# Kernel tuning notes

Measured on AMD Instinct MI355X. Metric: run time of the kernel, lower is better.

Reference implementation:

```python
import jax, jax.numpy as jnp
import numpy as np

HIDDEN = 2048
N_HEADS = 16
N_KV = 4
HEAD_DIM = 128
THETA = 500000.0
FREQ_ALLOC = 20  # t section; h = w = (HEAD_DIM//2 - 20)//2 = 22
T = 2048


def setup_inputs() -> dict:
    key = jax.random.key(0)
    k1, k2, k3, k4 = jax.random.split(key, 4)
    positions = jax.random.randint(k1, (3, T), 0, 1024, dtype=jnp.int32)
    hidden_states = jax.random.normal(k2, (T, HIDDEN), dtype=jnp.float32)
    w_qkv = jax.random.normal(k3, (HIDDEN, (N_HEADS + 2 * N_KV) * HEAD_DIM), dtype=jnp.float32) * 0.02
    w_o = jax.random.normal(k4, (N_HEADS * HEAD_DIM, HIDDEN), dtype=jnp.float32) * 0.02
    return {"positions": positions, "hidden_states": hidden_states, "w_qkv": w_qkv, "w_o": w_o}


def _mrope_cos_sin(positions):
    # standard rope table evaluated at positions: cos/sin each [3, T, HEAD_DIM//2]
    inv_freq = 1.0 / (THETA ** (jnp.arange(0, HEAD_DIM, 2, dtype=jnp.float32) / HEAD_DIM))
    freqs = positions.astype(jnp.float32)[..., None] * inv_freq
    cos, sin = jnp.cos(freqs), jnp.sin(freqs)
    sh = (HEAD_DIM // 2 - FREQ_ALLOC) // 2  # 22

    def section(c):
        c_t = c[0, :, -FREQ_ALLOC:]          # time dims from t-positions
        c_h = c[1, :, 0:2 * sh:2]            # even low-freq dims from h-positions
        c_w = c[2, :, 1:2 * sh:2]            # odd low-freq dims from w-positions
        c_hw = jnp.stack([c_h, c_w], axis=-1).reshape(c_h.shape[0], 2 * sh)
        return jnp.concatenate([c_hw, c_t], axis=-1)  # [T, HEAD_DIM//2]

    return section(cos), section(sin)


def _rotate_interleaved(x, cos, sin):
    # is_neox_style=False: even/odd interleaved rotation. x: [T, H, HEAD_DIM]
    x1, x2 = x[..., 0::2], x[..., 1::2]
    c, s = cos[:, None, :], sin[:, None, :]
    o1 = x1 * c - x2 * s
    o2 = x2 * c + x1 * s
    return jnp.stack([o1, o2], axis=-1).reshape(x.shape)


def reference(positions, hidden_states, w_qkv, w_o):
    q_size = N_HEADS * HEAD_DIM
    kv_size = N_KV * HEAD_DIM
    qkv = hidden_states @ w_qkv  # [T, 3072]
    q = qkv[:, :q_size].reshape(T, N_HEADS, HEAD_DIM)
    k = qkv[:, q_size:q_size + kv_size].reshape(T, N_KV, HEAD_DIM)
    v = qkv[:, q_size + kv_size:].reshape(T, N_KV, HEAD_DIM)

    cos, sin = _mrope_cos_sin(positions)
    q = _rotate_interleaved(q, cos, sin)
    k = _rotate_interleaved(k, cos, sin)

    # GQA causal attention
    rep = N_HEADS // N_KV
    kr = jnp.repeat(k, rep, axis=1)  # [T, N_HEADS, D]
    vr = jnp.repeat(v, rep, axis=1)
    scale = HEAD_DIM ** -0.5
    scores = jnp.einsum('qhd,khd->hqk', q, kr) * scale
    causal = jnp.tril(jnp.ones((T, T), dtype=bool))
    scores = jnp.where(causal[None], scores, jnp.finfo(scores.dtype).min)
    attn = jax.nn.softmax(scores, axis=-1)
    out = jnp.einsum('hqk,khd->qhd', attn, vr).reshape(T, N_HEADS * HEAD_DIM)
    return out @ w_o
```

## Files before the change

### kernel.cpp

```cpp
#include <hip/hip_runtime.h>
#include <math.h>

#define T 2048
#define HIDDEN 2048
#define NH 16
#define NKV 4
#define HD 128
#define QKV_N 3072
#define Q_SIZE 2048
#define KV_SIZE 512

typedef __attribute__((ext_vector_type(8))) short short8;
typedef __attribute__((ext_vector_type(4))) short short4v;
typedef __attribute__((ext_vector_type(4))) float floatx4;
typedef __attribute__((ext_vector_type(16))) float floatx16;

#define VMCNT(N) asm volatile("s_waitcnt vmcnt(" #N ")" ::: "memory")
#define LGKMCNT0 asm volatile("s_waitcnt lgkmcnt(0)" ::: "memory")
#define BARRIER_RAW()                          \
    do {                                       \
        __builtin_amdgcn_s_barrier();          \
        asm volatile("" ::: "memory");         \
    } while (0)

__device__ __forceinline__ unsigned short f2bf(float f) {
    union { float f; unsigned int u; } v; v.f = f;
    unsigned int u = v.u;
    u += 0x7fffu + ((u >> 16) & 1u);
    return (unsigned short)(u >> 16);
}

__device__ __forceinline__ void gload_lds16(const unsigned short* g, unsigned short* l) {
    __builtin_amdgcn_global_load_lds((const __attribute__((address_space(1))) unsigned int*)g,
                                     (__attribute__((address_space(3))) unsigned int*)l, 16, 0, 0);
}

__global__ __launch_bounds__(256) void prep_misc(const float* __restrict__ hidden,
                                                 const float* __restrict__ w_qkv,
                                                 const float* __restrict__ w_o,
                                                 const int* __restrict__ positions,
                                                 unsigned short* __restrict__ hb,
                                                 unsigned short* __restrict__ wqt,
                                                 unsigned short* __restrict__ wot,
                                                 float* __restrict__ cosT,
                                                 float* __restrict__ sinT) {
    __shared__ float tile[32][33];
    const int b = blockIdx.x;
    const int tid = threadIdx.x;
    const int tx = tid & 31, ty = tid >> 5;

    if (b < 4096) {
        int i = (b * 256 + tid) * 4;
        float4 v = *(const float4*)(hidden + i);
        hb[i]     = f2bf(v.x);
        hb[i + 1] = f2bf(v.y);
        hb[i + 2] = f2bf(v.z);
        hb[i + 3] = f2bf(v.w);
    } else if (b < 10240) {
        int idx = b - 4096;
        int c0 = (idx % 96) * 32, r0 = (idx / 96) * 32;
#pragma unroll
        for (int i = 0; i < 4; ++i)
            tile[ty + i * 8][tx] = w_qkv[(long)(r0 + ty + i * 8) * QKV_N + c0 + tx];
        __syncthreads();
#pragma unroll
        for (int i = 0; i < 4; ++i)
            wqt[(long)(c0 + ty + i * 8) * HIDDEN + r0 + tx] = f2bf(tile[tx][ty + i * 8]);
    } else if (b < 14336) {
        int idx = b - 10240;
        int c0 = (idx % 64) * 32, r0 = (idx / 64) * 32;
#pragma unroll
        for (int i = 0; i < 4; ++i)
            tile[ty + i * 8][tx] = w_o[(long)(r0 + ty + i * 8) * HIDDEN + c0 + tx];
        __syncthreads();
#pragma unroll
        for (int i = 0; i < 4; ++i)
            wot[(long)(c0 + ty + i * 8) * HIDDEN + r0 + tx] = f2bf(tile[tx][ty + i * 8]);
    } else {
        int idx = b - 14336;
        int t = idx * 4 + (tid >> 6);
        int j = tid & 63;
        int row = (j >= 44) ? 0 : ((j & 1) ? 2 : 1);
        int pos = positions[row * T + t];
        float invf = exp2f((float)j * -0.29580571f);
        float ang = (float)pos * invf;
        cosT[t * 64 + j] = cosf(ang);
        sinT[t * 64 + j] = sinf(ang);
    }
}

__global__ __launch_bounds__(256) void gemm_qkv(const unsigned short* __restrict__ A,
                                                const unsigned short* __restrict__ B,
                                                const float* __restrict__ cosT,
                                                const float* __restrict__ sinT,
                                                unsigned short* __restrict__ qb,
                                                unsigned short* __restrict__ kb,
                                                unsigned short* __restrict__ vt) {
    __shared__ __align__(16) unsigned short As[3][64 * 64];
    __shared__ __align__(16) unsigned short Bs[3][128 * 64];
    const int K = HIDDEN;
    const int tid = threadIdx.x;
    const int wv = tid >> 6;
    const int lane = tid & 63;
    const int m = lane & 15, qd = lane >> 4;
    const unsigned short* Ab = A + (long)(blockIdx.x * 64) * K;
    const unsigned short* Bb = B + (long)(blockIdx.y * 128) * K;

    floatx4 acc[4][2];
#pragma unroll
    for (int i = 0; i < 4; ++i)
#pragma unroll
        for (int j = 0; j < 2; ++j) acc[i][j] = (floatx4){0.f, 0.f, 0.f, 0.f};

#define QKV_STAGE(buf, k0)                                                                   \
    do {                                                                                     \
        _Pragma("unroll") for (int i_ = 0; i_ < 2; ++i_) {                                   \
            int s_ = i_ * 256 + tid, r_ = s_ >> 3, c_ = (s_ & 7) ^ (r_ & 7);                 \
            gload_lds16(Ab + (long)r_ * K + (k0) + c_ * 8, &As[buf][i_ * 2048 + wv * 512]);  \
        }                                                                                    \
        _Pragma("unroll") for (int i_ = 0; i_ < 4; ++i_) {                                   \
            int s_ = i_ * 256 + tid, r_ = s_ >> 3, c_ = (s_ & 7) ^ (r_ & 7);                 \
            gload_lds16(Bb + (long)r_ * K + (k0) + c_ * 8, &Bs[buf][i_ * 2048 + wv * 512]);  \
        }                                                                                    \
    } while (0)

    QKV_STAGE(0, 0);
    QKV_STAGE(1, 64);
    int cur = 0;
#pragma unroll 1
    for (int t = 0; t < 32; ++t) {
        if (t < 31) VMCNT(6); else VMCNT(0);
        BARRIER_RAW();
        if (t + 2 < 32) {
            int nb = cur + 2; if (nb >= 3) nb -= 3;
            QKV_STAGE(nb, (t + 2) * 64);
        }
#pragma unroll
        for (int kk = 0; kk < 2; ++kk) {
            const int rch = ((kk * 4 + qd) ^ (m & 7)) * 8;
            short8 a[4], b[2];
#pragma unroll
            for (int i = 0; i < 4; ++i) a[i] = *(const short8*)&As[cur][(i * 16 + m) * 64 + rch];
#pragma unroll
            for (int j = 0; j < 2; ++j) b[j] = *(const short8*)&Bs[cur][(wv * 32 + j * 16 + m) * 64 + rch];
#pragma unroll
            for (int i = 0; i < 4; ++i)
#pragma unroll
                for (int j = 0; j < 2; ++j)
                    acc[i][j] = __builtin_amdgcn_mfma_f32_16x16x32_bf16(a[i], b[j], acc[i][j], 0, 0, 0);
        }
        LGKMCNT0;
        cur = (cur == 2) ? 0 : cur + 1;
    }
#undef QKV_STAGE

    const int by = blockIdx.y;
    if (by < 20) {
        const float sgn = (m & 1) ? 1.f : -1.f;
        const float qscale = 0.08838834764831845f;
#pragma unroll
        for (int i = 0; i < 4; ++i) {
#pragma unroll
            for (int r = 0; r < 4; ++r) {
                const int t = blockIdx.x * 64 + i * 16 + qd * 4 + r;
                const float* ct = cosT + t * 64;
                const float* st = sinT + t * 64;
#pragma unroll
                for (int j = 0; j < 2; ++j) {
                    const int cq = wv * 32 + j * 16 + m;
                    const int j2 = cq >> 1;
                    float val = acc[i][j][r];
                    float prt = __shfl_xor(val, 1);
                    float o = val * ct[j2] + sgn * prt * st[j2];
                    const int col = by * 128 + cq;
                    if (by < 16) qb[(long)t * Q_SIZE + col] = f2bf(o * qscale);
                    else         kb[(long)t * KV_SIZE + (col - 2048)] = f2bf(o);
                }
            }
        }
    } else {
        const int g = by - 20;
#pragma unroll
        for (int i = 0; i < 4; ++i)
#pragma unroll
            for (int j = 0; j < 2; ++j) {
                const int d = wv * 32 + j * 16 + m;
                const int t0 = blockIdx.x * 64 + i * 16 + qd * 4;
                unsigned short o4[4];
#pragma unroll
                for (int r = 0; r < 4; ++r) o4[r] = f2bf(acc[i][j][r]);
                *(short4v*)&vt[((long)g * HD + d) * T + t0] = *(short4v*)o4;
            }
    }
}

__global__ __launch_bounds__(256) void gemm_out(const unsigned short* __restrict__ A,
                                                const unsigned short* __restrict__ B,
                                                float* __restrict__ C,
                                                int K, int ldc) {
    __shared__ __align__(16) unsigned short Ls[3][256 * 64];
    const int tid = threadIdx.x;
    const int wv = tid >> 6;
    const int lane = tid & 63;
    const int l31 = lane & 31;
    const int hi = lane >> 5;
    const int wr = wv >> 1, wc = wv & 1;
    const int by = blockIdx.x;
    const int bx = blockIdx.y;
    const unsigned short* Ab = A + (long)(bx * 128) * K;
    const unsigned short* Bb = B + (long)(by * 128) * K;

    floatx16 acc[2][2];
#pragma unroll
    for (int i = 0; i < 2; ++i)
#pragma unroll
        for (int j = 0; j < 2; ++j) acc[i][j] = (floatx16)0.0f;

#define OUT_STAGE(bufidx, k0)                                                          \
    do {                                                                               \
        unsigned short* lb_ = &Ls[bufidx][0];                                          \
        _Pragma("unroll") for (int qq_ = 0; qq_ < 8; ++qq_) {                          \
            int q_ = qq_ * 4 + wv;                                                     \
            int s_ = q_ * 64 + lane;                                                   \
            int r_ = s_ >> 3;                                                          \
            int c_ = (s_ & 7) ^ (r_ & 7);                                              \
            const unsigned short* src_ = (q_ < 16)                                     \
                ? (Ab + (long)r_ * K + (k0) + c_ * 8)                                  \
                : (Bb + (long)(r_ - 128) * K + (k0) + c_ * 8);                         \
            gload_lds16(src_, lb_ + q_ * 512);                                         \
        }                                                                              \
    } while (0)

    const int NT = K >> 6;
    OUT_STAGE(0, 0);
    OUT_STAGE(1, 64);
    int cur = 0;
    const int arow0 = wr * 64 + l31;
    const int brow0 = 128 + wc * 64 + l31;
#pragma unroll 1
    for (int t = 0; t < NT; ++t) {
        if (t < NT - 1) VMCNT(8); else VMCNT(0);
        BARRIER_RAW();
        if (t + 2 < NT) {
            int nb = cur + 2; if (nb >= 3) nb -= 3;
            OUT_STAGE(nb, (t + 2) * 64);
        }
        const unsigned short* lb = &Ls[cur][0];
#pragma unroll
        for (int kk = 0; kk < 4; ++kk) {
            const int ck = kk * 2 + hi;
            short8 a[2], b[2];
#pragma unroll
            for (int i = 0; i < 2; ++i) {
                const int row = arow0 + i * 32;
                a[i] = *(const short8*)&lb[row * 64 + ((ck ^ (row & 7)) << 3)];
            }
#pragma unroll
            for (int j = 0; j < 2; ++j) {
                const int row = brow0 + j * 32;
                b[j] = *(const short8*)&lb[row * 64 + ((ck ^ (row & 7)) << 3)];
            }
#pragma unroll
            for (int i = 0; i < 2; ++i)
#pragma unroll
                for (int j = 0; j < 2; ++j)
                    acc[i][j] = __builtin_amdgcn_mfma_f32_32x32x16_bf16(a[i], b[j], acc[i][j], 0, 0, 0);
        }
        LGKMCNT0;
        cur = (cur == 2) ? 0 : cur + 1;
    }
#undef OUT_STAGE

#pragma unroll
    for (int i = 0; i < 2; ++i)
#pragma unroll
        for (int j = 0; j < 2; ++j) {
            const long rbase = (long)(bx * 128 + wr * 64 + i * 32 + 4 * hi);
            const int cbase = by * 128 + wc * 64 + j * 32 + l31;
#pragma unroll
            for (int h = 0; h < 4; ++h)
#pragma unroll
                for (int r = 0; r < 4; ++r)
                    C[(rbase + 8 * h + r) * ldc + cbase] = acc[i][j][h * 4 + r];
        }
}

__global__ __launch_bounds__(256, 2) void flash_attn(const unsigned short* __restrict__ qb,
                                                     const unsigned short* __restrict__ kb,
                                                     const unsigned short* __restrict__ vt,
                                                     float* __restrict__ Opart,
                                                     float* __restrict__ MLpart) {
    __shared__ __align__(16) unsigned short Kbuf[2][64 * 128];
    __shared__ __align__(16) unsigned short Vbuf[128 * 64];
    __shared__ __align__(16) unsigned short Pls[4][32 * 72];

    const int tid = threadIdx.x;
    const int wv = tid >> 6;
    const int lane = tid & 63;
    const int m = lane & 15;
    const int qd = lane >> 4;

    const int bx = blockIdx.x;
    const int c_ = bx & 255;
    const int hi = bx >> 8;
    const int h = c_ >> 4;
    const int j_ = c_ & 15;
    const int qt = hi ? (j_ >> 1) : (15 - (j_ >> 1));
    const int half = j_ & 1;
    const int g = h >> 2;
    unsigned short* myP = Pls[wv];

    const int n0 = qt + 1;
    const int jt0 = half ? n0 : 0;
    const int jt1 = half ? 2 * qt + 2 : n0;
    const int q0 = qt * 128;

    short8 aq[2][4];
#pragma unroll
    for (int s = 0; s < 2; ++s)
#pragma unroll
        for (int kk = 0; kk < 4; ++kk)
            aq[s][kk] = *(const short8*)(qb + (long)(q0 + s * 64 + wv * 16 + m) * Q_SIZE +
                                         h * HD + kk * 32 + qd * 8);

    floatx4 acc_o[2][8];
#pragma unroll
    for (int s = 0; s < 2; ++s)
#pragma unroll
        for (int nb = 0; nb < 8; ++nb) acc_o[s][nb] = (floatx4){0.f, 0.f, 0.f, 0.f};
    float mrow[2] = {-1e30f, -1e30f};
    float lrow[2] = {0.f, 0.f};

#pragma unroll
    for (int i = 0; i < 4; ++i) {
        int s_ = i * 256 + tid;
        int r = s_ >> 4, c = (s_ & 15) ^ (r & 15);
        gload_lds16(kb + (long)(jt0 * 64 + r) * KV_SIZE + g * HD + c * 8,
                    &Kbuf[0][i * 2048 + wv * 512]);
    }
    int cur = 0;
    for (int jt = jt0; jt < jt1; ++jt) {
        VMCNT(0);
        BARRIER_RAW();

#pragma unroll
        for (int i = 0; i < 4; ++i) {
            int s_ = i * 256 + tid;
            int r = s_ >> 3, c = (s_ & 7) ^ (r & 7);
            gload_lds16(vt + ((long)g * HD + r) * T + jt * 64 + c * 8,
                        &Vbuf[i * 2048 + wv * 512]);
        }
        const bool pk = (jt + 1 < jt1);
        if (pk) {
#pragma unroll
            for (int i = 0; i < 4; ++i) {
                int s_ = i * 256 + tid;
                int r = s_ >> 4, c = (s_ & 15) ^ (r & 15);
                gload_lds16(kb + (long)((jt + 1) * 64 + r) * KV_SIZE + g * HD + c * 8,
                            &Kbuf[cur ^ 1][i * 2048 + wv * 512]);
            }
        }

        floatx4 acc_s[2][4];
#pragma unroll
        for (int s = 0; s < 2; ++s)
#pragma unroll
            for (int c = 0; c < 4; ++c) acc_s[s][c] = (floatx4){0.f, 0.f, 0.f, 0.f};
#pragma unroll
        for (int kk = 0; kk < 4; ++kk) {
#pragma unroll
            for (int c = 0; c < 4; ++c) {
                short8 ak = *(const short8*)&Kbuf[cur][(c * 16 + m) * 128 +
                                                       (((4 * kk + qd) ^ m) * 8)];
                acc_s[0][c] = __builtin_amdgcn_mfma_f32_16x16x32_bf16(ak, aq[0][kk], acc_s[0][c], 0, 0, 0);
                acc_s[1][c] = __builtin_amdgcn_mfma_f32_16x16x32_bf16(ak, aq[1][kk], acc_s[1][c], 0, 0, 0);
            }
        }

#pragma unroll
        for (int s = 0; s < 2; ++s) {
            const int dg = 2 * qt + s;
            if (jt >= dg) {
                const bool full = (jt > dg);
#pragma unroll
                for (int c = 0; c < 4; ++c)
#pragma unroll
                    for (int r = 0; r < 4; ++r)
                        if (full || (c * 16 + qd * 4 + r > wv * 16 + m)) acc_s[s][c][r] = -1e30f;
            }
            float mx = acc_s[s][0][0];
#pragma unroll
            for (int c = 0; c < 4; ++c)
#pragma unroll
                for (int r = 0; r < 4; ++r) mx = fmaxf(mx, acc_s[s][c][r]);
            mx = fmaxf(mx, __shfl_xor(mx, 16));
            mx = fmaxf(mx, __shfl_xor(mx, 32));
            float mnew = fmaxf(mrow[s], mx);
            float alpha = __expf(mrow[s] - mnew);
            mrow[s] = mnew;

            float pv[4][4];
            float lsum = 0.f;
#pragma unroll
            for (int c = 0; c < 4; ++c)
#pragma unroll
                for (int r = 0; r < 4; ++r) {
                    pv[c][r] = __expf(acc_s[s][c][r] - mnew);
                    lsum += pv[c][r];
                }
            lsum += __shfl_xor(lsum, 16);
            lsum += __shfl_xor(lsum, 32);
            lrow[s] = lrow[s] * alpha + lsum;
#pragma unroll
            for (int nb = 0; nb < 8; ++nb)
#pragma unroll
                for (int r = 0; r < 4; ++r) acc_o[s][nb][r] *= alpha;
#pragma unroll
            for (int c = 0; c < 4; ++c) {
                short4v pk2 = {(short)f2bf(pv[c][0]), (short)f2bf(pv[c][1]),
                               (short)f2bf(pv[c][2]), (short)f2bf(pv[c][3])};
                *(short4v*)&myP[(s * 16 + m) * 72 + c * 16 + qd * 4] = pk2;
            }
        }

        if (pk) VMCNT(4); else VMCNT(0);
        BARRIER_RAW();

#pragma unroll
        for (int kk = 0; kk < 2; ++kk) {
            short8 pa0 = *(const short8*)&myP[m * 72 + kk * 32 + qd * 8];
            short8 pa1 = *(const short8*)&myP[(16 + m) * 72 + kk * 32 + qd * 8];
#pragma unroll
            for (int nb = 0; nb < 8; ++nb) {
                short8 av = *(const short8*)&Vbuf[(nb * 16 + m) * 64 +
                                                  (((4 * kk + qd) ^ (m & 7)) * 8)];
                acc_o[0][nb] = __builtin_amdgcn_mfma_f32_16x16x32_bf16(av, pa0, acc_o[0][nb], 0, 0, 0);
                acc_o[1][nb] = __builtin_amdgcn_mfma_f32_16x16x32_bf16(av, pa1, acc_o[1][nb], 0, 0, 0);
            }
        }
        LGKMCNT0;
        cur ^= 1;
    }

    const int unit = (h * 16 + qt) * 2 + half;
#pragma unroll
    for (int s = 0; s < 2; ++s) {
        const long rb = (long)unit * 128 + s * 64 + wv * 16 + m;
#pragma unroll
        for (int nb = 0; nb < 8; ++nb)
            *(floatx4*)&Opart[rb * 128 + nb * 16 + qd * 4] = acc_o[s][nb];
        if (qd == 0) {
            MLpart[rb * 2]     = mrow[s];
            MLpart[rb * 2 + 1] = lrow[s];
        }
    }
}

__global__ __launch_bounds__(256) void attn_combine(const float* __restrict__ Opart,
                                                    const float* __restrict__ MLpart,
                                                    unsigned short* __restrict__ ab) {
    const int tid = threadIdx.x;
    const int q = blockIdx.x * 16 + (tid >> 4);
    const int h = blockIdx.y;
    const int d0 = (tid & 15) * 8;
    const int qt = q >> 7, lr = q & 127;
    const long r0 = ((long)(h * 16 + qt) * 2) * 128 + lr;
    const long r1 = r0 + 128;
    float m0 = MLpart[r0 * 2], l0 = MLpart[r0 * 2 + 1];
    float m1 = MLpart[r1 * 2], l1 = MLpart[r1 * 2 + 1];
    float M = fmaxf(m0, m1);
    float a0 = __expf(m0 - M), a1 = __expf(m1 - M);
    float inv = 1.f / (l0 * a0 + l1 * a1);
    const float* O0 = Opart + r0 * 128 + d0;
    const float* O1 = Opart + r1 * 128 + d0;
    unsigned short outv[8];
#pragma unroll
    for (int j = 0; j < 8; j += 4) {
        float4 x0 = *(const float4*)(O0 + j);
        float4 x1 = *(const float4*)(O1 + j);
        outv[j]     = f2bf((x0.x * a0 + x1.x * a1) * inv);
        outv[j + 1] = f2bf((x0.y * a0 + x1.y * a1) * inv);
        outv[j + 2] = f2bf((x0.z * a0 + x1.z * a1) * inv);
        outv[j + 3] = f2bf((x0.w * a0 + x1.w * a1) * inv);
    }
    *(short8*)&ab[(long)q * Q_SIZE + h * HD + d0] = *(short8*)outv;
}

extern "C" void kernel_launch(void* const* d_in, const int* in_sizes, int n_in,
                              void* d_out, int out_size, void* d_ws, size_t ws_size,
                              hipStream_t stream) {
    const int* positions = (const int*)d_in[0];
    const float* hidden  = (const float*)d_in[1];
    const float* w_qkv   = (const float*)d_in[2];
    const float* w_o     = (const float*)d_in[3];
    float* out = (float*)d_out;

    char* p = (char*)d_ws;
    auto alloc = [&](size_t bytes) { char* r = p; p += (bytes + 255) & ~(size_t)255; return r; };
    float* cosT = (float*)alloc((size_t)T * 64 * 4);
    float* sinT = (float*)alloc((size_t)T * 64 * 4);
    unsigned short* hb  = (unsigned short*)alloc((size_t)T * HIDDEN * 2);
    unsigned short* wqt = (unsigned short*)alloc((size_t)QKV_N * HIDDEN * 2);
    unsigned short* wot = (unsigned short*)alloc((size_t)HIDDEN * HIDDEN * 2);
    unsigned short* qb  = (unsigned short*)alloc((size_t)T * Q_SIZE * 2);
    unsigned short* kb  = (unsigned short*)alloc((size_t)T * KV_SIZE * 2);
    unsigned short* vt  = (unsigned short*)alloc((size_t)T * KV_SIZE * 2);
    unsigned short* ab  = (unsigned short*)alloc((size_t)T * Q_SIZE * 2);
    float* Opart  = (float*)alloc((size_t)512 * 128 * 128 * 4);
    float* MLpart = (float*)alloc((size_t)512 * 128 * 2 * 4);

    prep_misc<<<dim3(14848), 256, 0, stream>>>(hidden, w_qkv, w_o, positions,
                                               hb, wqt, wot, cosT, sinT);
    gemm_qkv<<<dim3(T / 64, QKV_N / 128), 256, 0, stream>>>(hb, wqt, cosT, sinT, qb, kb, vt);
    flash_attn<<<dim3(512), 256, 0, stream>>>(qb, kb, vt, Opart, MLpart);
    attn_combine<<<dim3(T / 16, NH), 256, 0, stream>>>(Opart, MLpart, ab);
    gemm_out<<<dim3(HIDDEN / 128, T / 128), 256, 0, stream>>>(ab, wot, out, Q_SIZE, HIDDEN);
}
```

Measured before the change: 238.8 us.

## Drop split-KV attention with combine kernel; use 64-row query tiles and double buffering

Flash attention now gives each block a 64-row query tile over its full causal key range, instead of two blocks each covering half the keys of a 128-row tile. This removes the partial-output buffers and the separate combine kernel, and the normalized bf16 output is written directly. The cost is less work per block and less reuse of K/V tiles, plus uneven causal work per block, balanced only by the hi/lo ordering. The QKV GEMM also moves from a three-stage pipeline with explicit waitcnt to a simpler two-buffer loop with __syncthreads, which may expose more load latency.

```diff
diff --git a/kernel.cpp b/kernel.cpp
--- a/kernel.cpp
+++ b/kernel.cpp
@@ -96,8 +96,8 @@
                                                 unsigned short* __restrict__ qb,
                                                 unsigned short* __restrict__ kb,
                                                 unsigned short* __restrict__ vt) {
-    __shared__ __align__(16) unsigned short As[3][64 * 64];
-    __shared__ __align__(16) unsigned short Bs[3][128 * 64];
+    __shared__ __align__(16) unsigned short As[2][64 * 64];
+    __shared__ __align__(16) unsigned short Bs[2][128 * 64];
     const int K = HIDDEN;
     const int tid = threadIdx.x;
     const int wv = tid >> 6;
@@ -125,16 +125,10 @@
     } while (0)
 
     QKV_STAGE(0, 0);
-    QKV_STAGE(1, 64);
     int cur = 0;
-#pragma unroll 1
-    for (int t = 0; t < 32; ++t) {
-        if (t < 31) VMCNT(6); else VMCNT(0);
-        BARRIER_RAW();
-        if (t + 2 < 32) {
-            int nb = cur + 2; if (nb >= 3) nb -= 3;
-            QKV_STAGE(nb, (t + 2) * 64);
-        }
+    for (int k0 = 0; k0 < K; k0 += 64) {
+        __syncthreads();
+        if (k0 + 64 < K) QKV_STAGE(cur ^ 1, k0 + 64);
 #pragma unroll
         for (int kk = 0; kk < 2; ++kk) {
             const int rch = ((kk * 4 + qd) ^ (m & 7)) * 8;
@@ -149,8 +143,7 @@
                 for (int j = 0; j < 2; ++j)
                     acc[i][j] = __builtin_amdgcn_mfma_f32_16x16x32_bf16(a[i], b[j], acc[i][j], 0, 0, 0);
         }
-        LGKMCNT0;
-        cur = (cur == 2) ? 0 : cur + 1;
+        cur ^= 1;
     }
 #undef QKV_STAGE
 
@@ -288,11 +281,10 @@
 __global__ __launch_bounds__(256, 2) void flash_attn(const unsigned short* __restrict__ qb,
                                                      const unsigned short* __restrict__ kb,
                                                      const unsigned short* __restrict__ vt,
-                                                     float* __restrict__ Opart,
-                                                     float* __restrict__ MLpart) {
+                                                     unsigned short* __restrict__ ab) {
     __shared__ __align__(16) unsigned short Kbuf[2][64 * 128];
     __shared__ __align__(16) unsigned short Vbuf[128 * 64];
-    __shared__ __align__(16) unsigned short Pls[4][32 * 72];
+    __shared__ __align__(16) unsigned short Pls[4][16 * 72];
 
     const int tid = threadIdx.x;
     const int wv = tid >> 6;
@@ -305,41 +297,33 @@
     const int hi = bx >> 8;
     const int h = c_ >> 4;
     const int j_ = c_ & 15;
-    const int qt = hi ? (j_ >> 1) : (15 - (j_ >> 1));
-    const int half = j_ & 1;
+    const int qt2 = hi ? j_ : (31 - j_);
     const int g = h >> 2;
     unsigned short* myP = Pls[wv];
 
-    const int n0 = qt + 1;
-    const int jt0 = half ? n0 : 0;
-    const int jt1 = half ? 2 * qt + 2 : n0;
-    const int q0 = qt * 128;
-
-    short8 aq[2][4];
-#pragma unroll
-    for (int s = 0; s < 2; ++s)
-#pragma unroll
-        for (int kk = 0; kk < 4; ++kk)
-            aq[s][kk] = *(const short8*)(qb + (long)(q0 + s * 64 + wv * 16 + m) * Q_SIZE +
-                                         h * HD + kk * 32 + qd * 8);
-
-    floatx4 acc_o[2][8];
-#pragma unroll
-    for (int s = 0; s < 2; ++s)
-#pragma unroll
-        for (int nb = 0; nb < 8; ++nb) acc_o[s][nb] = (floatx4){0.f, 0.f, 0.f, 0.f};
-    float mrow[2] = {-1e30f, -1e30f};
-    float lrow[2] = {0.f, 0.f};
+    const int jt1 = qt2 + 1;
+    const int qrow = qt2 * 64 + wv * 16 + m;
+
+    short8 aq[4];
+#pragma unroll
+    for (int kk = 0; kk < 4; ++kk)
+        aq[kk] = *(const short8*)(qb + (long)qrow * Q_SIZE + h * HD + kk * 32 + qd * 8);
+
+    floatx4 acc_o[8];
+#pragma unroll
+    for (int nb = 0; nb < 8; ++nb) acc_o[nb] = (floatx4){0.f, 0.f, 0.f, 0.f};
+    float mrow = -1e30f;
+    float lrow = 0.f;
 
 #pragma unroll
     for (int i = 0; i < 4; ++i) {
         int s_ = i * 256 + tid;
         int r = s_ >> 4, c = (s_ & 15) ^ (r & 15);
-        gload_lds16(kb + (long)(jt0 * 64 + r) * KV_SIZE + g * HD + c * 8,
+        gload_lds16(kb + (long)r * KV_SIZE + g * HD + c * 8,
                     &Kbuf[0][i * 2048 + wv * 512]);
     }
     int cur = 0;
-    for (int jt = jt0; jt < jt1; ++jt) {
+    for (int jt = 0; jt < jt1; ++jt) {
         VMCNT(0);
         BARRIER_RAW();
 
@@ -361,66 +345,59 @@
             }
         }
 
-        floatx4 acc_s[2][4];
-#pragma unroll
-        for (int s = 0; s < 2; ++s)
-#pragma unroll
-            for (int c = 0; c < 4; ++c) acc_s[s][c] = (floatx4){0.f, 0.f, 0.f, 0.f};
+        floatx4 acc_s[4];
+#pragma unroll
+        for (int c = 0; c < 4; ++c) acc_s[c] = (floatx4){0.f, 0.f, 0.f, 0.f};
 #pragma unroll
         for (int kk = 0; kk < 4; ++kk) {
 #pragma unroll
             for (int c = 0; c < 4; ++c) {
                 short8 ak = *(const short8*)&Kbuf[cur][(c * 16 + m) * 128 +
                                                        (((4 * kk + qd) ^ m) * 8)];
-                acc_s[0][c] = __builtin_amdgcn_mfma_f32_16x16x32_bf16(ak, aq[0][kk], acc_s[0][c], 0, 0, 0);
-                acc_s[1][c] = __builtin_amdgcn_mfma_f32_16x16x32_bf16(ak, aq[1][kk], acc_s[1][c], 0, 0, 0);
-            }
-        }
-
-#pragma unroll
-        for (int s = 0; s < 2; ++s) {
-            const int dg = 2 * qt + s;
-            if (jt >= dg) {
-                const bool full = (jt > dg);
-#pragma unroll
-                for (int c = 0; c < 4; ++c)
-#pragma unroll
-                    for (int r = 0; r < 4; ++r)
-                        if (full || (c * 16 + qd * 4 + r > wv * 16 + m)) acc_s[s][c][r] = -1e30f;
-            }
-            float mx = acc_s[s][0][0];
+                acc_s[c] = __builtin_amdgcn_mfma_f32_16x16x32_bf16(ak, aq[kk], acc_s[c], 0, 0, 0);
+            }
+        }
+
+        if (jt == qt2) {
 #pragma unroll
             for (int c = 0; c < 4; ++c)
 #pragma unroll
-                for (int r = 0; r < 4; ++r) mx = fmaxf(mx, acc_s[s][c][r]);
-            mx = fmaxf(mx, __shfl_xor(mx, 16));
-            mx = fmaxf(mx, __shfl_xor(mx, 32));
-            float mnew = fmaxf(mrow[s], mx);
-            float alpha = __expf(mrow[s] - mnew);
-            mrow[s] = mnew;
-
-            float pv[4][4];
-            float lsum = 0.f;
-#pragma unroll
-            for (int c = 0; c < 4; ++c)
-#pragma unroll
-                for (int r = 0; r < 4; ++r) {
-                    pv[c][r] = __expf(acc_s[s][c][r] - mnew);
-                    lsum += pv[c][r];
-                }
-            lsum += __shfl_xor(lsum, 16);
-            lsum += __shfl_xor(lsum, 32);
-            lrow[s] = lrow[s] * alpha + lsum;
-#pragma unroll
-            for (int nb = 0; nb < 8; ++nb)
-#pragma unroll
-                for (int r = 0; r < 4; ++r) acc_o[s][nb][r] *= alpha;
-#pragma unroll
-            for (int c = 0; c < 4; ++c) {
-                short4v pk2 = {(short)f2bf(pv[c][0]), (short)f2bf(pv[c][1]),
-                               (short)f2bf(pv[c][2]), (short)f2bf(pv[c][3])};
-                *(short4v*)&myP[(s * 16 + m) * 72 + c * 16 + qd * 4] = pk2;
-            }
+                for (int r = 0; r < 4; ++r)
+                    if (c * 16 + qd * 4 + r > wv * 16 + m) acc_s[c][r] = -1e30f;
+        }
+
+        float mx = acc_s[0][0];
+#pragma unroll
+        for (int c = 0; c < 4; ++c)
+#pragma unroll
+            for (int r = 0; r < 4; ++r) mx = fmaxf(mx, acc_s[c][r]);
+        mx = fmaxf(mx, __shfl_xor(mx, 16));
+        mx = fmaxf(mx, __shfl_xor(mx, 32));
+        float mnew = fmaxf(mrow, mx);
+        float alpha = __expf(mrow - mnew);
+        mrow = mnew;
+
+        float pv[4][4];
+        float lsum = 0.f;
+#pragma unroll
+        for (int c = 0; c < 4; ++c)
+#pragma unroll
+            for (int r = 0; r < 4; ++r) {
+                pv[c][r] = __expf(acc_s[c][r] - mnew);
+                lsum += pv[c][r];
+            }
+        lsum += __shfl_xor(lsum, 16);
+        lsum += __shfl_xor(lsum, 32);
+        lrow = lrow * alpha + lsum;
+#pragma unroll
+        for (int nb = 0; nb < 8; ++nb)
+#pragma unroll
+            for (int r = 0; r < 4; ++r) acc_o[nb][r] *= alpha;
+#pragma unroll
+        for (int c = 0; c < 4; ++c) {
+            short4v pk2 = {(short)f2bf(pv[c][0]), (short)f2bf(pv[c][1]),
+                           (short)f2bf(pv[c][2]), (short)f2bf(pv[c][3])};
+            *(short4v*)&myP[m * 72 + c * 16 + qd * 4] = pk2;
         }
 
         if (pk) VMCNT(4); else VMCNT(0);
@@ -428,62 +405,26 @@
 
 #pragma unroll
         for (int kk = 0; kk < 2; ++kk) {
-            short8 pa0 = *(const short8*)&myP[m * 72 + kk * 32 + qd * 8];
-            short8 pa1 = *(const short8*)&myP[(16 + m) * 72 + kk * 32 + qd * 8];
+            short8 pa = *(const short8*)&myP[m * 72 + kk * 32 + qd * 8];
 #pragma unroll
             for (int nb = 0; nb < 8; ++nb) {
                 short8 av = *(const short8*)&Vbuf[(nb * 16 + m) * 64 +
                                                   (((4 * kk + qd) ^ (m & 7)) * 8)];
-                acc_o[0][nb] = __builtin_amdgcn_mfma_f32_16x16x32_bf16(av, pa0, acc_o[0][nb], 0, 0, 0);
-                acc_o[1][nb] = __builtin_amdgcn_mfma_f32_16x16x32_bf16(av, pa1, acc_o[1][nb], 0, 0, 0);
+                acc_o[nb] = __builtin_amdgcn_mfma_f32_16x16x32_bf16(av, pa, acc_o[nb], 0, 0, 0);
             }
         }
         LGKMCNT0;
         cur ^= 1;
     }
 
-    const int unit = (h * 16 + qt) * 2 + half;
-#pragma unroll
-    for (int s = 0; s < 2; ++s) {
-        const long rb = (long)unit * 128 + s * 64 + wv * 16 + m;
-#pragma unroll
-        for (int nb = 0; nb < 8; ++nb)
-            *(floatx4*)&Opart[rb * 128 + nb * 16 + qd * 4] = acc_o[s][nb];
-        if (qd == 0) {
-            MLpart[rb * 2]     = mrow[s];
-            MLpart[rb * 2 + 1] = lrow[s];
-        }
-    }
-}
-
-__global__ __launch_bounds__(256) void attn_combine(const float* __restrict__ Opart,
-                                                    const float* __restrict__ MLpart,
-                                                    unsigned short* __restrict__ ab) {
-    const int tid = threadIdx.x;
-    const int q = blockIdx.x * 16 + (tid >> 4);
-    const int h = blockIdx.y;
-    const int d0 = (tid & 15) * 8;
-    const int qt = q >> 7, lr = q & 127;
-    const long r0 = ((long)(h * 16 + qt) * 2) * 128 + lr;
-    const long r1 = r0 + 128;
-    float m0 = MLpart[r0 * 2], l0 = MLpart[r0 * 2 + 1];
-    float m1 = MLpart[r1 * 2], l1 = MLpart[r1 * 2 + 1];
-    float M = fmaxf(m0, m1);
-    float a0 = __expf(m0 - M), a1 = __expf(m1 - M);
-    float inv = 1.f / (l0 * a0 + l1 * a1);
-    const float* O0 = Opart + r0 * 128 + d0;
-    const float* O1 = Opart + r1 * 128 + d0;
-    unsigned short outv[8];
-#pragma unroll
-    for (int j = 0; j < 8; j += 4) {
-        float4 x0 = *(const float4*)(O0 + j);
-        float4 x1 = *(const float4*)(O1 + j);
-        outv[j]     = f2bf((x0.x * a0 + x1.x * a1) * inv);
-        outv[j + 1] = f2bf((x0.y * a0 + x1.y * a1) * inv);
-        outv[j + 2] = f2bf((x0.z * a0 + x1.z * a1) * inv);
-        outv[j + 3] = f2bf((x0.w * a0 + x1.w * a1) * inv);
-    }
-    *(short8*)&ab[(long)q * Q_SIZE + h * HD + d0] = *(short8*)outv;
+    const float inv = 1.f / lrow;
+#pragma unroll
+    for (int nb = 0; nb < 8; ++nb) {
+        unsigned short o4[4];
+#pragma unroll
+        for (int r = 0; r < 4; ++r) o4[r] = f2bf(acc_o[nb][r] * inv);
+        *(short4v*)&ab[(long)qrow * Q_SIZE + h * HD + nb * 16 + qd * 4] = *(short4v*)o4;
+    }
 }
 
 extern "C" void kernel_launch(void* const* d_in, const int* in_sizes, int n_in,
@@ -506,13 +447,10 @@
     unsigned short* kb  = (unsigned short*)alloc((size_t)T * KV_SIZE * 2);
     unsigned short* vt  = (unsigned short*)alloc((size_t)T * KV_SIZE * 2);
     unsigned short* ab  = (unsigned short*)alloc((size_t)T * Q_SIZE * 2);
-    float* Opart  = (float*)alloc((size_t)512 * 128 * 128 * 4);
-    float* MLpart = (float*)alloc((size_t)512 * 128 * 2 * 4);
 
     prep_misc<<<dim3(14848), 256, 0, stream>>>(hidden, w_qkv, w_o, positions,
                                                hb, wqt, wot, cosT, sinT);
     gemm_qkv<<<dim3(T / 64, QKV_N / 128), 256, 0, stream>>>(hb, wqt, cosT, sinT, qb, kb, vt);
-    flash_attn<<<dim3(512), 256, 0, stream>>>(qb, kb, vt, Opart, MLpart);
-    attn_combine<<<dim3(T / 16, NH), 256, 0, stream>>>(Opart, MLpart, ab);
+    flash_attn<<<dim3(512), 256, 0, stream>>>(qb, kb, vt, ab);
     gemm_out<<<dim3(HIDDEN / 128, T / 128), 256, 0, stream>>>(ab, wot, out, Q_SIZE, HIDDEN);
 }
```

Result: faster. 219.2 us (-8.2%).

## Split only heavy causal query tiles in attention and write light tiles directly

Applied to the files above, without the earlier changes.

Flash attention now splits the KV range into two halves only for the upper eight query tiles. The lower eight tiles run unsplit and normalise and write bf16 output straight into the attention buffer, which shrinks the partial buffers and the combine launch to the upper half. This cuts partial-result traffic and combine work, but leaves uneven block durations. Separately, the QKV GEMM drops from a three-stage pipeline with explicit vmcnt waits to a simpler double buffer synchronised by __syncthreads, which may expose more load latency.

```diff
diff --git a/kernel.cpp b/kernel.cpp
--- a/kernel.cpp
+++ b/kernel.cpp
@@ -96,8 +96,8 @@
                                                 unsigned short* __restrict__ qb,
                                                 unsigned short* __restrict__ kb,
                                                 unsigned short* __restrict__ vt) {
-    __shared__ __align__(16) unsigned short As[3][64 * 64];
-    __shared__ __align__(16) unsigned short Bs[3][128 * 64];
+    __shared__ __align__(16) unsigned short As[2][64 * 64];
+    __shared__ __align__(16) unsigned short Bs[2][128 * 64];
     const int K = HIDDEN;
     const int tid = threadIdx.x;
     const int wv = tid >> 6;
@@ -125,16 +125,10 @@
     } while (0)
 
     QKV_STAGE(0, 0);
-    QKV_STAGE(1, 64);
     int cur = 0;
-#pragma unroll 1
-    for (int t = 0; t < 32; ++t) {
-        if (t < 31) VMCNT(6); else VMCNT(0);
-        BARRIER_RAW();
-        if (t + 2 < 32) {
-            int nb = cur + 2; if (nb >= 3) nb -= 3;
-            QKV_STAGE(nb, (t + 2) * 64);
-        }
+    for (int k0 = 0; k0 < K; k0 += 64) {
+        __syncthreads();
+        if (k0 + 64 < K) QKV_STAGE(cur ^ 1, k0 + 64);
 #pragma unroll
         for (int kk = 0; kk < 2; ++kk) {
             const int rch = ((kk * 4 + qd) ^ (m & 7)) * 8;
@@ -149,8 +143,7 @@
                 for (int j = 0; j < 2; ++j)
                     acc[i][j] = __builtin_amdgcn_mfma_f32_16x16x32_bf16(a[i], b[j], acc[i][j], 0, 0, 0);
         }
-        LGKMCNT0;
-        cur = (cur == 2) ? 0 : cur + 1;
+        cur ^= 1;
     }
 #undef QKV_STAGE
 
@@ -288,6 +281,7 @@
 __global__ __launch_bounds__(256, 2) void flash_attn(const unsigned short* __restrict__ qb,
                                                      const unsigned short* __restrict__ kb,
                                                      const unsigned short* __restrict__ vt,
+                                                     unsigned short* __restrict__ ab,
                                                      float* __restrict__ Opart,
                                                      float* __restrict__ MLpart) {
     __shared__ __align__(16) unsigned short Kbuf[2][64 * 128];
@@ -301,18 +295,24 @@
     const int qd = lane >> 4;
 
     const int bx = blockIdx.x;
-    const int c_ = bx & 255;
-    const int hi = bx >> 8;
-    const int h = c_ >> 4;
-    const int j_ = c_ & 15;
-    const int qt = hi ? (j_ >> 1) : (15 - (j_ >> 1));
-    const int half = j_ & 1;
+    const bool heavy = (bx < 256);
+    int h, qt, half;
+    if (heavy) {
+        h = bx >> 4;
+        const int j_ = bx & 15;
+        qt = 15 - (j_ >> 1);
+        half = j_ & 1;
+    } else {
+        const int idx = bx - 256;
+        h = idx & 15;
+        qt = 7 - (idx >> 4);
+        half = 0;
+    }
     const int g = h >> 2;
     unsigned short* myP = Pls[wv];
 
-    const int n0 = qt + 1;
-    const int jt0 = half ? n0 : 0;
-    const int jt1 = half ? 2 * qt + 2 : n0;
+    const int jt0 = (heavy && half) ? qt + 1 : 0;
+    const int jt1 = (heavy && !half) ? qt + 1 : 2 * qt + 2;
     const int q0 = qt * 128;
 
     short8 aq[2][4];
@@ -442,16 +442,31 @@
         cur ^= 1;
     }
 
-    const int unit = (h * 16 + qt) * 2 + half;
-#pragma unroll
-    for (int s = 0; s < 2; ++s) {
-        const long rb = (long)unit * 128 + s * 64 + wv * 16 + m;
-#pragma unroll
-        for (int nb = 0; nb < 8; ++nb)
-            *(floatx4*)&Opart[rb * 128 + nb * 16 + qd * 4] = acc_o[s][nb];
-        if (qd == 0) {
-            MLpart[rb * 2]     = mrow[s];
-            MLpart[rb * 2 + 1] = lrow[s];
+    if (heavy) {
+        const int unit = (h * 8 + (qt - 8)) * 2 + half;
+#pragma unroll
+        for (int s = 0; s < 2; ++s) {
+            const long rb = (long)unit * 128 + s * 64 + wv * 16 + m;
+#pragma unroll
+            for (int nb = 0; nb < 8; ++nb)
+                *(floatx4*)&Opart[rb * 128 + nb * 16 + qd * 4] = acc_o[s][nb];
+            if (qd == 0) {
+                MLpart[rb * 2]     = mrow[s];
+                MLpart[rb * 2 + 1] = lrow[s];
+            }
+        }
+    } else {
+#pragma unroll
+        for (int s = 0; s < 2; ++s) {
+            const float inv = 1.f / lrow[s];
+            const long qrow = q0 + s * 64 + wv * 16 + m;
+#pragma unroll
+            for (int nb = 0; nb < 8; ++nb) {
+                unsigned short o4[4];
+#pragma unroll
+                for (int r = 0; r < 4; ++r) o4[r] = f2bf(acc_o[s][nb][r] * inv);
+                *(short4v*)&ab[qrow * Q_SIZE + h * HD + nb * 16 + qd * 4] = *(short4v*)o4;
+            }
         }
     }
 }
@@ -460,11 +475,11 @@
                                                     const float* __restrict__ MLpart,
                                                     unsigned short* __restrict__ ab) {
     const int tid = threadIdx.x;
-    const int q = blockIdx.x * 16 + (tid >> 4);
+    const int q = 1024 + blockIdx.x * 16 + (tid >> 4);
     const int h = blockIdx.y;
     const int d0 = (tid & 15) * 8;
     const int qt = q >> 7, lr = q & 127;
-    const long r0 = ((long)(h * 16 + qt) * 2) * 128 + lr;
+    const long r0 = ((long)(h * 8 + (qt - 8)) * 2) * 128 + lr;
     const long r1 = r0 + 128;
     float m0 = MLpart[r0 * 2], l0 = MLpart[r0 * 2 + 1];
     float m1 = MLpart[r1 * 2], l1 = MLpart[r1 * 2 + 1];
@@ -506,13 +521,13 @@
     unsigned short* kb  = (unsigned short*)alloc((size_t)T * KV_SIZE * 2);
     unsigned short* vt  = (unsigned short*)alloc((size_t)T * KV_SIZE * 2);
     unsigned short* ab  = (unsigned short*)alloc((size_t)T * Q_SIZE * 2);
-    float* Opart  = (float*)alloc((size_t)512 * 128 * 128 * 4);
-    float* MLpart = (float*)alloc((size_t)512 * 128 * 2 * 4);
+    float* Opart  = (float*)alloc((size_t)256 * 128 * 128 * 4);
+    float* MLpart = (float*)alloc((size_t)256 * 128 * 2 * 4);
 
     prep_misc<<<dim3(14848), 256, 0, stream>>>(hidden, w_qkv, w_o, positions,
                                                hb, wqt, wot, cosT, sinT);
     gemm_qkv<<<dim3(T / 64, QKV_N / 128), 256, 0, stream>>>(hb, wqt, cosT, sinT, qb, kb, vt);
-    flash_attn<<<dim3(512), 256, 0, stream>>>(qb, kb, vt, Opart, MLpart);
-    attn_combine<<<dim3(T / 16, NH), 256, 0, stream>>>(Opart, MLpart, ab);
+    flash_attn<<<dim3(384), 256, 0, stream>>>(qb, kb, vt, ab, Opart, MLpart);
+    attn_combine<<<dim3(64, NH), 256, 0, stream>>>(Opart, MLpart, ab);
     gemm_out<<<dim3(HIDDEN / 128, T / 128), 256, 0, stream>>>(ab, wot, out, Q_SIZE, HIDDEN);
 }
```

Result: faster. 224.8 us (-5.9%).

## Fuse attention split-combine into flash_attn via atomic counters; simplify QKV GEMM pipeline

Applied to the files above, without the earlier changes.

Removes the separate attn_combine kernel: each flash_attn block increments a per-(head,q-tile) counter, and the block that finishes second merges both partial outputs and writes bf16 attention output. The QKV GEMM is switched from a 3-stage vmcnt-controlled pipeline to a simpler 2-stage double buffer with __syncthreads, which also zeroes the flags. This saves a kernel launch and a pass over the partials, but it risks less latency hiding in the GEMM and depends on correct memory fencing for the atomic handoff.

```diff
diff --git a/kernel.cpp b/kernel.cpp
--- a/kernel.cpp
+++ b/kernel.cpp
@@ -95,9 +95,10 @@
                                                 const float* __restrict__ sinT,
                                                 unsigned short* __restrict__ qb,
                                                 unsigned short* __restrict__ kb,
-                                                unsigned short* __restrict__ vt) {
-    __shared__ __align__(16) unsigned short As[3][64 * 64];
-    __shared__ __align__(16) unsigned short Bs[3][128 * 64];
+                                                unsigned short* __restrict__ vt,
+                                                int* __restrict__ flags) {
+    __shared__ __align__(16) unsigned short As[2][64 * 64];
+    __shared__ __align__(16) unsigned short Bs[2][128 * 64];
     const int K = HIDDEN;
     const int tid = threadIdx.x;
     const int wv = tid >> 6;
@@ -105,6 +106,8 @@
     const int m = lane & 15, qd = lane >> 4;
     const unsigned short* Ab = A + (long)(blockIdx.x * 64) * K;
     const unsigned short* Bb = B + (long)(blockIdx.y * 128) * K;
+
+    if (blockIdx.x == 0 && blockIdx.y == 0) flags[tid] = 0;
 
     floatx4 acc[4][2];
 #pragma unroll
@@ -125,16 +128,10 @@
     } while (0)
 
     QKV_STAGE(0, 0);
-    QKV_STAGE(1, 64);
     int cur = 0;
-#pragma unroll 1
-    for (int t = 0; t < 32; ++t) {
-        if (t < 31) VMCNT(6); else VMCNT(0);
-        BARRIER_RAW();
-        if (t + 2 < 32) {
-            int nb = cur + 2; if (nb >= 3) nb -= 3;
-            QKV_STAGE(nb, (t + 2) * 64);
-        }
+    for (int k0 = 0; k0 < K; k0 += 64) {
+        __syncthreads();
+        if (k0 + 64 < K) QKV_STAGE(cur ^ 1, k0 + 64);
 #pragma unroll
         for (int kk = 0; kk < 2; ++kk) {
             const int rch = ((kk * 4 + qd) ^ (m & 7)) * 8;
@@ -149,8 +146,7 @@
                 for (int j = 0; j < 2; ++j)
                     acc[i][j] = __builtin_amdgcn_mfma_f32_16x16x32_bf16(a[i], b[j], acc[i][j], 0, 0, 0);
         }
-        LGKMCNT0;
-        cur = (cur == 2) ? 0 : cur + 1;
+        cur ^= 1;
     }
 #undef QKV_STAGE
 
@@ -288,8 +284,10 @@
 __global__ __launch_bounds__(256, 2) void flash_attn(const unsigned short* __restrict__ qb,
                                                      const unsigned short* __restrict__ kb,
                                                      const unsigned short* __restrict__ vt,
+                                                     unsigned short* __restrict__ ab,
                                                      float* __restrict__ Opart,
-                                                     float* __restrict__ MLpart) {
+                                                     float* __restrict__ MLpart,
+                                                     int* __restrict__ flags) {
     __shared__ __align__(16) unsigned short Kbuf[2][64 * 128];
     __shared__ __align__(16) unsigned short Vbuf[128 * 64];
     __shared__ __align__(16) unsigned short Pls[4][32 * 72];
@@ -442,7 +440,8 @@
         cur ^= 1;
     }
 
-    const int unit = (h * 16 + qt) * 2 + half;
+    const int u2 = h * 16 + qt;
+    const int unit = u2 * 2 + half;
 #pragma unroll
     for (int s = 0; s < 2; ++s) {
         const long rb = (long)unit * 128 + s * 64 + wv * 16 + m;
@@ -454,36 +453,40 @@
             MLpart[rb * 2 + 1] = lrow[s];
         }
     }
-}
-
-__global__ __launch_bounds__(256) void attn_combine(const float* __restrict__ Opart,
-                                                    const float* __restrict__ MLpart,
-                                                    unsigned short* __restrict__ ab) {
-    const int tid = threadIdx.x;
-    const int q = blockIdx.x * 16 + (tid >> 4);
-    const int h = blockIdx.y;
-    const int d0 = (tid & 15) * 8;
-    const int qt = q >> 7, lr = q & 127;
-    const long r0 = ((long)(h * 16 + qt) * 2) * 128 + lr;
-    const long r1 = r0 + 128;
-    float m0 = MLpart[r0 * 2], l0 = MLpart[r0 * 2 + 1];
-    float m1 = MLpart[r1 * 2], l1 = MLpart[r1 * 2 + 1];
-    float M = fmaxf(m0, m1);
-    float a0 = __expf(m0 - M), a1 = __expf(m1 - M);
-    float inv = 1.f / (l0 * a0 + l1 * a1);
-    const float* O0 = Opart + r0 * 128 + d0;
-    const float* O1 = Opart + r1 * 128 + d0;
-    unsigned short outv[8];
-#pragma unroll
-    for (int j = 0; j < 8; j += 4) {
-        float4 x0 = *(const float4*)(O0 + j);
-        float4 x1 = *(const float4*)(O1 + j);
-        outv[j]     = f2bf((x0.x * a0 + x1.x * a1) * inv);
-        outv[j + 1] = f2bf((x0.y * a0 + x1.y * a1) * inv);
-        outv[j + 2] = f2bf((x0.z * a0 + x1.z * a1) * inv);
-        outv[j + 3] = f2bf((x0.w * a0 + x1.w * a1) * inv);
-    }
-    *(short8*)&ab[(long)q * Q_SIZE + h * HD + d0] = *(short8*)outv;
+
+    __syncthreads();
+    __shared__ int amLastSh;
+    if (tid == 0) {
+        __threadfence();
+        amLastSh = (atomicAdd(&flags[u2], 1) == 1);
+    }
+    __syncthreads();
+    if (amLastSh) {
+        __threadfence();
+        const int row = tid >> 1;
+        const int c0 = (tid & 1) * 64;
+        const long r0 = (long)(u2 * 2) * 128 + row;
+        const long r1 = r0 + 128;
+        float m0 = MLpart[r0 * 2], l0 = MLpart[r0 * 2 + 1];
+        float m1 = MLpart[r1 * 2], l1 = MLpart[r1 * 2 + 1];
+        float M = fmaxf(m0, m1);
+        float a0 = __expf(m0 - M), a1 = __expf(m1 - M);
+        float inv = 1.f / (l0 * a0 + l1 * a1);
+        const float* O0 = Opart + r0 * 128 + c0;
+        const float* O1 = Opart + r1 * 128 + c0;
+        unsigned short* dst = ab + (long)(q0 + row) * Q_SIZE + h * HD + c0;
+#pragma unroll
+        for (int j = 0; j < 64; j += 4) {
+            float4 x0 = *(const float4*)(O0 + j);
+            float4 x1 = *(const float4*)(O1 + j);
+            unsigned short ov[4];
+            ov[0] = f2bf((x0.x * a0 + x1.x * a1) * inv);
+            ov[1] = f2bf((x0.y * a0 + x1.y * a1) * inv);
+            ov[2] = f2bf((x0.z * a0 + x1.z * a1) * inv);
+            ov[3] = f2bf((x0.w * a0 + x1.w * a1) * inv);
+            *(short4v*)(dst + j) = *(short4v*)ov;
+        }
+    }
 }
 
 extern "C" void kernel_launch(void* const* d_in, const int* in_sizes, int n_in,
@@ -508,11 +511,11 @@
     unsigned short* ab  = (unsigned short*)alloc((size_t)T * Q_SIZE * 2);
     float* Opart  = (float*)alloc((size_t)512 * 128 * 128 * 4);
     float* MLpart = (float*)alloc((size_t)512 * 128 * 2 * 4);
+    int*   flags  = (int*)alloc(256 * 4);
 
     prep_misc<<<dim3(14848), 256, 0, stream>>>(hidden, w_qkv, w_o, positions,
                                                hb, wqt, wot, cosT, sinT);
-    gemm_qkv<<<dim3(T / 64, QKV_N / 128), 256, 0, stream>>>(hb, wqt, cosT, sinT, qb, kb, vt);
-    flash_attn<<<dim3(512), 256, 0, stream>>>(qb, kb, vt, Opart, MLpart);
-    attn_combine<<<dim3(T / 16, NH), 256, 0, stream>>>(Opart, MLpart, ab);
+    gemm_qkv<<<dim3(T / 64, QKV_N / 128), 256, 0, stream>>>(hb, wqt, cosT, sinT, qb, kb, vt, flags);
+    flash_attn<<<dim3(512), 256, 0, stream>>>(qb, kb, vt, ab, Opart, MLpart, flags);
     gemm_out<<<dim3(HIDDEN / 128, T / 128), 256, 0, stream>>>(ab, wot, out, Q_SIZE, HIDDEN);
 }
```

After: 292.1 us. 22.3% more time.
